# Kernel tuning notes

Measured on AMD Instinct MI355X. Metric: run time of the kernel, lower is better.

## Reference

```python
import jax, jax.numpy as jnp
import numpy as np

TRIANGLE_TABLE = jnp.array([
    [-1, -1, -1, -1, -1, -1], [1, 0, 2, -1, -1, -1], [4, 0, 3, -1, -1, -1],
    [1, 4, 2, 1, 3, 4], [3, 1, 5, -1, -1, -1], [2, 3, 0, 2, 5, 3],
    [1, 4, 0, 1, 5, 4], [4, 2, 5, -1, -1, -1], [4, 5, 2, -1, -1, -1],
    [4, 1, 0, 4, 5, 1], [3, 2, 0, 3, 5, 2], [1, 3, 5, -1, -1, -1],
    [4, 1, 2, 4, 3, 1], [3, 0, 4, -1, -1, -1], [2, 0, 1, -1, -1, -1],
    [-1, -1, -1, -1, -1, -1]], dtype=jnp.int32)
NUM_TRI_TABLE = jnp.array([0, 1, 1, 2, 1, 2, 2, 1, 1, 2, 2, 1, 2, 1, 1, 0], dtype=jnp.int32)
BASE_TET_EDGES = jnp.array([0, 1, 0, 2, 0, 3, 1, 2, 1, 3, 2, 3], dtype=jnp.int32)

NUM_VERTS = 500_000
NUM_TETS = 2_000_000


def setup_inputs() -> dict:
    key = jax.random.key(0)
    k1, k2, k3 = jax.random.split(key, 3)
    pos_nx3 = jax.random.normal(k1, (NUM_VERTS, 3), dtype=jnp.float32)
    sdf_n = jax.random.normal(k2, (NUM_VERTS,), dtype=jnp.float32)
    tet_fx4 = jax.random.randint(k3, (NUM_TETS, 4), 0, NUM_VERTS)
    return {"pos_nx3": pos_nx3, "sdf_n": sdf_n, "tet_fx4": tet_fx4}


def _map_uv(face_gidx, max_idx):
    N = int(np.ceil(np.sqrt((max_idx + 1) // 2)))
    lin = jnp.linspace(0.0, 1.0 - 1.0 / N, N, dtype=jnp.float32)
    tex_y, tex_x = jnp.meshgrid(lin, lin, indexing='ij')
    pad = 0.9 / N
    # (N, N, 8) -> (N*N*4, 2): 4 uv corners per texel
    uvs = jnp.stack([tex_x, tex_y, tex_x + pad, tex_y,
                     tex_x + pad, tex_y + pad, tex_x, tex_y + pad], axis=-1).reshape(-1, 2)
    tet_idx = face_gidx // 2
    x = tet_idx % N
    y = tet_idx // N
    tet_idx = y * N + x
    tri_idx = face_gidx % 2
    uv_idx = jnp.stack([tet_idx * 4, tet_idx * 4 + tri_idx + 1,
                        tet_idx * 4 + tri_idx + 2], axis=-1).reshape(-1, 3)
    return uvs, uv_idx


def reference(pos_nx3, sdf_n, tet_fx4):
    # --- topology extraction (non-differentiable, data-dependent shapes; eager) ---
    occ_n = sdf_n > 0                                  # (N,)
    occ_fx4 = occ_n[tet_fx4]                           # (F, 4)
    occ_sum = occ_fx4.sum(-1)
    valid = (occ_sum > 0) & (occ_sum < 4)              # surface-crossing tets
    tets_v = tet_fx4[valid]                            # (Fv, 4)

    e = tets_v[:, BASE_TET_EDGES].reshape(-1, 2)       # (Fv*6, 2)
    e = jnp.stack([jnp.minimum(e[:, 0], e[:, 1]),
                   jnp.maximum(e[:, 0], e[:, 1])], axis=-1)  # sorted edges
    unique_edges, idx_map = jnp.unique(e, axis=0, return_inverse=True)
    idx_map = idx_map.reshape(-1)

    mask_edges = occ_n[unique_edges].sum(-1) == 1      # edges crossing surface
    mapping = jnp.where(mask_edges, jnp.cumsum(mask_edges) - 1, -1)
    idx_map = mapping[idx_map].reshape(-1, 6)          # (Fv, 6) per-tet edge->vert id
    interp_v = unique_edges[mask_edges]                # (E, 2)

    # --- differentiable vertex interpolation ---
    p = pos_nx3[interp_v]                              # (E, 2, 3)
    signs = jnp.array([[1.0], [-1.0]], dtype=pos_nx3.dtype)
    s = sdf_n[interp_v][..., None] * signs             # (E, 2, 1), second negated
    w = jnp.flip(s, axis=1) / s.sum(1, keepdims=True)
    verts = (p * w).sum(1)                             # (E, 3)

    # --- triangulation via lookup table ---
    v_id = jnp.array([1, 2, 4, 8], dtype=jnp.int32)
    tetindex = (occ_fx4[valid].astype(jnp.int32) * v_id).sum(-1)  # (Fv,)
    ntri = NUM_TRI_TABLE[tetindex]
    m1 = ntri == 1
    m2 = ntri == 2
    f1 = jnp.take_along_axis(idx_map[m1], TRIANGLE_TABLE[tetindex[m1]][:, :3], axis=1).reshape(-1, 3)
    f2 = jnp.take_along_axis(idx_map[m2], TRIANGLE_TABLE[tetindex[m2]][:, :6], axis=1).reshape(-1, 3)
    faces = jnp.concatenate([f1, f2], axis=0)

    num_tets = tet_fx4.shape[0]
    tet_gidx = jnp.arange(num_tets)[valid]
    g2 = tet_gidx[m2] * 2
    face_gidx = jnp.concatenate([tet_gidx[m1] * 2,
                                 jnp.stack([g2, g2 + 1], axis=-1).reshape(-1)], axis=0)
    uvs, uv_idx = _map_uv(face_gidx, num_tets * 2)
    return verts, faces, uvs, uv_idx
```

## Files before the change

kernel.cpp:

```cpp
#include <hip/hip_runtime.h>
#include <stdint.h>
#include <math.h>

#define SB 256
#define SI 8
#define SCHUNK (SB*SI)
#define C2 2048
#define LDSN (C2 + 256)
#define HEADBIT 0x40000000u
#define VMASK   0x3FFFFFFFu

__constant__ int c_tri[16][6] = {
  {-1,-1,-1,-1,-1,-1},{1,0,2,-1,-1,-1},{4,0,3,-1,-1,-1},{1,4,2,1,3,4},
  {3,1,5,-1,-1,-1},{2,3,0,2,5,3},{1,4,0,1,5,4},{4,2,5,-1,-1,-1},
  {4,5,2,-1,-1,-1},{4,1,0,4,5,1},{3,2,0,3,5,2},{1,3,5,-1,-1,-1},
  {4,1,2,4,3,1},{3,0,4,-1,-1,-1},{2,0,1,-1,-1,-1},{-1,-1,-1,-1,-1,-1}};
__constant__ int c_ntri[16] = {0,1,1,2,1,2,2,1,1,2,2,1,2,1,1,0};
__constant__ int c_ea[6] = {0,0,0,1,1,2};
__constant__ int c_eb[6] = {1,2,3,2,3,3};

__global__ void k_classify(const int4* __restrict__ tet, const float* __restrict__ sdf,
                           uint8_t* __restrict__ tetidx, int* __restrict__ bucketCnt,
                           ushort4* __restrict__ stash, int nt) {
  int t = blockIdx.x * blockDim.x + threadIdx.x;
  if (t >= nt) return;
  int4 v = tet[t];
  int ids[4] = {v.x, v.y, v.z, v.w};
  int bits = 0;
#pragma unroll
  for (int i = 0; i < 4; i++) bits |= (sdf[ids[i]] > 0.0f) ? (1 << i) : 0;
  tetidx[t] = (uint8_t)bits;
  if (c_ntri[bits] == 0) return;
  int los[4];
  int c = 0;
#pragma unroll
  for (int e = 0; e < 6; e++) {
    int a = c_ea[e], b = c_eb[e];
    if ((((bits >> a) ^ (bits >> b)) & 1) == 0) continue;
    int va = ids[a], vb = ids[b];
    los[c++] = va < vb ? va : vb;
  }
  unsigned short st[4] = {0, 0, 0, 0};
  unsigned done = 0;
#pragma unroll
  for (int i = 0; i < 4; i++) {
    if (i >= c || (done & (1u << i))) continue;
    int cnt = 1;
#pragma unroll
    for (int j = 1; j < 4; j++)
      if (i + j < c && los[i + j] == los[i]) cnt++;
    int base = atomicAdd(&bucketCnt[los[i]], cnt);
    int k = 0;
#pragma unroll
    for (int j = 0; j < 4; j++) {
      if (i + j < c && los[i + j] == los[i]) {
        st[i + j] = (unsigned short)(base + k);
        k++;
        done |= 1u << (i + j);
      }
    }
  }
  stash[t] = make_ushort4(st[0], st[1], st[2], st[3]);
}

__device__ inline unsigned long long blkExclU64(unsigned long long val, unsigned long long* sh) {
  int tid = threadIdx.x;
  sh[tid] = val; __syncthreads();
  for (int st = 1; st < SB; st <<= 1) {
    unsigned long long add = (tid >= st) ? sh[tid - st] : 0ull;
    __syncthreads();
    sh[tid] += add;
    __syncthreads();
  }
  return sh[tid] - val;
}
__device__ inline int blkExclI32(int val, int* sh) {
  int tid = threadIdx.x;
  sh[tid] = val; __syncthreads();
  for (int st = 1; st < SB; st <<= 1) {
    int add = (tid >= st) ? sh[tid - st] : 0;
    __syncthreads();
    sh[tid] += add;
    __syncthreads();
  }
  return sh[tid] - val;
}

__global__ void k_pass1(const uint8_t* __restrict__ tetidx, int nt,
                        const int* __restrict__ bucketCnt, int nv,
                        unsigned long long* __restrict__ btU, int* __restrict__ btI, int nb_t) {
  __shared__ unsigned long long shU[SB];
  int* shI = (int*)shU;
  if ((int)blockIdx.x < nb_t) {
    int base = blockIdx.x * SCHUNK + threadIdx.x * SI;
    unsigned long long s = 0;
    for (int k = 0; k < SI; k++) {
      int i = base + k;
      if (i < nt) {
        int n3 = c_ntri[tetidx[i]];
        s += (n3 == 1 ? 1ull : 0ull) + (n3 == 2 ? (1ull << 32) : 0ull);
      }
    }
    shU[threadIdx.x] = s; __syncthreads();
    for (int st = SB / 2; st > 0; st >>= 1) {
      if (threadIdx.x < st) shU[threadIdx.x] += shU[threadIdx.x + st];
      __syncthreads();
    }
    if (threadIdx.x == 0) btU[blockIdx.x] = shU[0];
  } else {
    int bid = blockIdx.x - nb_t;
    int base = bid * SCHUNK + threadIdx.x * SI;
    int s = 0;
    for (int k = 0; k < SI; k++) { int i = base + k; if (i < nv) s += bucketCnt[i]; }
    shI[threadIdx.x] = s; __syncthreads();
    for (int st = SB / 2; st > 0; st >>= 1) {
      if (threadIdx.x < st) shI[threadIdx.x] += shI[threadIdx.x + st];
      __syncthreads();
    }
    if (threadIdx.x == 0) btI[bid] = shI[0];
  }
}

__global__ void k_scanmid(unsigned long long* __restrict__ btU, int nbU,
                          int* __restrict__ btI, int nbI, int* __restrict__ scal) {
  __shared__ unsigned long long shU[SB];
  __shared__ unsigned long long carryU;
  int* shI = (int*)shU;
  __shared__ int carryI;
  if (blockIdx.x == 0) {
    if (threadIdx.x == 0) carryU = 0;
    __syncthreads();
    for (int base = 0; base < nbU; base += SB) {
      int i = base + threadIdx.x;
      unsigned long long v = (i < nbU) ? btU[i] : 0ull;
      unsigned long long ex = blkExclU64(v, shU);
      unsigned long long carry = carryU;
      if (i < nbU) btU[i] = carry + ex;
      __syncthreads();
      if (threadIdx.x == SB - 1) carryU = carry + ex + v;
      __syncthreads();
    }
    if (threadIdx.x == 0) {
      scal[0] = (int)(carryU & 0xffffffffull);
      scal[1] = (int)(carryU >> 32);
    }
  } else {
    if (threadIdx.x == 0) carryI = 0;
    __syncthreads();
    for (int base = 0; base < nbI; base += SB) {
      int i = base + threadIdx.x;
      int v = (i < nbI) ? btI[i] : 0;
      int ex = blkExclI32(v, shI);
      int carry = carryI;
      if (i < nbI) btI[i] = carry + ex;
      __syncthreads();
      if (threadIdx.x == SB - 1) carryI = carry + ex + v;
      __syncthreads();
    }
    if (threadIdx.x == 0) scal[2] = carryI;
  }
}

__global__ void k_pass3(const uint8_t* __restrict__ tetidx, int nt,
                        const int* __restrict__ bucketCnt, int nv,
                        const unsigned long long* __restrict__ btU, const int* __restrict__ btI,
                        const int* __restrict__ scal,
                        unsigned* __restrict__ rowIdx, int* __restrict__ bucketOff,
                        int nb_t) {
  __shared__ unsigned long long shU[SB];
  int* shI = (int*)shU;
  if ((int)blockIdx.x < nb_t) {
    int M1 = scal[0];
    int base = blockIdx.x * SCHUNK + threadIdx.x * SI;
    unsigned long long vals[SI];
    int n3s[SI];
    unsigned long long s = 0;
    for (int k = 0; k < SI; k++) {
      int i = base + k;
      unsigned long long v = 0;
      int n3 = 0;
      if (i < nt) {
        n3 = c_ntri[tetidx[i]];
        v = (n3 == 1 ? 1ull : 0ull) + (n3 == 2 ? (1ull << 32) : 0ull);
      }
      n3s[k] = n3;
      vals[k] = s; s += v;
    }
    unsigned long long thrOff = blkExclU64(s, shU);
    unsigned long long off = btU[blockIdx.x] + thrOff;
    for (int k = 0; k < SI; k++) {
      int i = base + k;
      if (i < nt) {
        unsigned long long r = off + vals[k];
        unsigned row = (n3s[k] == 1) ? (unsigned)(r & 0xffffffffull)
                                     : (unsigned)(M1 + 2 * (int)(r >> 32));
        rowIdx[i] = row;
      }
    }
  } else {
    int bid = blockIdx.x - nb_t;
    int base = bid * SCHUNK + threadIdx.x * SI;
    int vals[SI];
    int s = 0;
    for (int k = 0; k < SI; k++) {
      int i = base + k;
      int v = (i < nv) ? bucketCnt[i] : 0;
      vals[k] = s; s += v;
    }
    int thrOff = blkExclI32(s, shI);
    int off = btI[bid] + thrOff;
    for (int k = 0; k < SI; k++) {
      int i = base + k;
      if (i < nv) bucketOff[i] = off + vals[k];
    }
  }
}

__global__ void k_i32scan1(const int* __restrict__ src, int* __restrict__ bt, int n) {
  __shared__ int sh[SB];
  int base = blockIdx.x * SCHUNK + threadIdx.x * SI;
  int s = 0;
  for (int k = 0; k < SI; k++) { int i = base + k; if (i < n) s += src[i]; }
  sh[threadIdx.x] = s; __syncthreads();
  for (int st = SB / 2; st > 0; st >>= 1) {
    if (threadIdx.x < st) sh[threadIdx.x] += sh[threadIdx.x + st];
    __syncthreads();
  }
  if (threadIdx.x == 0) bt[blockIdx.x] = sh[0];
}

__global__ void k_uscanblk(int* __restrict__ bt, int nb, int* __restrict__ scal, int uvsElems) {
  __shared__ int sh[SB];
  __shared__ int carrySh;
  if (threadIdx.x == 0) carrySh = 0;
  __syncthreads();
  for (int base = 0; base < nb; base += SB) {
    int i = base + threadIdx.x;
    int v = (i < nb) ? bt[i] : 0;
    int ex = blkExclI32(v, sh);
    int carry = carrySh;
    if (i < nb) bt[i] = carry + ex;
    __syncthreads();
    if (threadIdx.x == SB - 1) carrySh = carry + ex + v;
    __syncthreads();
  }
  if (threadIdx.x == 0) {
    int E = carrySh;
    scal[3] = E;
    int M1 = scal[0], M2 = scal[1];
    int F = M1 + 2 * M2;
    scal[4] = 3 * E;
    scal[5] = 3 * E + 3 * F;
    scal[6] = scal[5] + uvsElems;
  }
}

__global__ void k_i32scan3(const int* __restrict__ src, const int* __restrict__ bt,
                           int* __restrict__ dst, int n) {
  __shared__ int sh[SB];
  int base = blockIdx.x * SCHUNK + threadIdx.x * SI;
  int vals[SI];
  int s = 0;
  for (int k = 0; k < SI; k++) {
    int i = base + k;
    int v = (i < n) ? src[i] : 0;
    vals[k] = s; s += v;
  }
  int thrOff = blkExclI32(s, sh);
  int off = bt[blockIdx.x] + thrOff;
  for (int k = 0; k < SI; k++) {
    int i = base + k;
    if (i < n) dst[i] = off + vals[k];
  }
}

__global__ void k_scatter(const int4* __restrict__ tet, const uint8_t* __restrict__ tetidx,
                          const int* __restrict__ bucketOff, const ushort4* __restrict__ stash,
                          unsigned* __restrict__ edges32, int4* __restrict__ stashAbs, int nt) {
  int t = blockIdx.x * blockDim.x + threadIdx.x;
  if (t >= nt) return;
  int bits = tetidx[t];
  if (c_ntri[bits] == 0) return;
  int4 v = tet[t];
  int ids[4] = {v.x, v.y, v.z, v.w};
  ushort4 stv = stash[t];
  unsigned short sta[4] = {stv.x, stv.y, stv.z, stv.w};
  int sa[4] = {0, 0, 0, 0};
  int c = 0;
#pragma unroll
  for (int e = 0; e < 6; e++) {
    int a = c_ea[e], b = c_eb[e];
    if ((((bits >> a) ^ (bits >> b)) & 1) == 0) continue;
    int va = ids[a], vb = ids[b];
    int lo = va < vb ? va : vb;
    int hi = va < vb ? vb : va;
    int abs = bucketOff[lo] + (int)sta[c];
    edges32[abs] = (unsigned)hi;
    sa[c] = abs;
    c++;
  }
  stashAbs[t] = make_int4(sa[0], sa[1], sa[2], sa[3]);
}

__global__ __launch_bounds__(SB) void k_rankuniq(
    const int* __restrict__ bucketOff, const unsigned* __restrict__ edges32,
    unsigned short* __restrict__ hrankArr, unsigned* __restrict__ edgesU,
    int* __restrict__ uniqueCnt, int* __restrict__ tmpHead,
    const int* __restrict__ scal, int nv) {
  __shared__ unsigned sh[LDSN];
  __shared__ unsigned shB[LDSN];
  __shared__ int shVS, shVE;
  int totSlots = scal[2];
  long long s0 = (long long)blockIdx.x * C2;
  long long s1 = s0 + C2;
  if (threadIdx.x == 0) {
    int lo = 0, hi = nv;
    while (lo < hi) { int mid = (lo + hi) >> 1;
      long long key = (long long)bucketOff[mid] + mid;
      if (key < s0) lo = mid + 1; else hi = mid; }
    shVS = lo;
    hi = nv;
    while (lo < hi) { int mid = (lo + hi) >> 1;
      long long key = (long long)bucketOff[mid] + mid;
      if (key < s1) lo = mid + 1; else hi = mid; }
    shVE = lo;
  }
  __syncthreads();
  int vS = shVS, vE = shVE;
  if (vS >= vE) return;
  int occS = bucketOff[vS];
  int occE = (vE < nv) ? bucketOff[vE] : totSlots;
  int cnt = occE - occS;
  if (cnt <= LDSN) {
    for (int v = vS + threadIdx.x; v < vE; v += SB) {
      int o = bucketOff[v];
      int nx = (v + 1 < nv) ? bucketOff[v + 1] : totSlots;
      if (nx > o) {
        unsigned pack = ((unsigned)(o - occS) << 16) | (unsigned)(nx - occS);
        for (int k = o; k < nx; k++) shB[k - occS] = pack;
      }
    }
    for (int i = threadIdx.x; i < cnt; i += SB) sh[i] = edges32[occS + i];
    __syncthreads();
    for (int i = threadIdx.x; i < cnt; i += SB) {
      int lb = (int)(shB[i] >> 16);
      unsigned myv = sh[i] & VMASK;
      bool head = true;
      for (int k = lb; k < i; k++)
        if (((sh[k] ^ myv) & VMASK) == 0) { head = false; break; }
      if (head) sh[i] = myv | HEADBIT;
    }
    __syncthreads();
    for (int i = threadIdx.x; i < cnt; i += SB) {
      unsigned b = shB[i];
      int lb = (int)(b >> 16), le = (int)(b & 0xffffu);
      unsigned w0 = sh[i];
      unsigned myv = w0 & VMASK;
      int rank = 0;
      for (int k = lb; k < le; k++) {
        unsigned w = sh[k];
        rank += ((w & HEADBIT) != 0u && (w & VMASK) < myv) ? 1 : 0;
      }
      hrankArr[occS + i] = (unsigned short)rank;
      if (w0 & HEADBIT) edgesU[occS + lb + rank] = myv;
    }
    for (int v = vS + threadIdx.x; v < vE; v += SB) {
      int o = bucketOff[v];
      int nx = (v + 1 < nv) ? bucketOff[v + 1] : totSlots;
      int u = 0;
      for (int k = o - occS; k < nx - occS; k++) u += (sh[k] & HEADBIT) ? 1 : 0;
      uniqueCnt[v] = u;
    }
  } else {
    for (int v = vS + threadIdx.x; v < vE; v += SB) {
      int o = bucketOff[v];
      int nx = (v + 1 < nv) ? bucketOff[v + 1] : totSlots;
      int n = nx - o;
      if (n <= 0) { uniqueCnt[v] = 0; continue; }
      for (int j = 0; j < n; j++) {
        unsigned myv = edges32[o + j];
        int head = 1;
        for (int k = 0; k < j; k++) if (edges32[o + k] == myv) { head = 0; break; }
        tmpHead[o + j] = head;
      }
      int u = 0;
      for (int j = 0; j < n; j++) {
        unsigned myv = edges32[o + j];
        int rank = 0;
        for (int k = 0; k < n; k++)
          rank += (tmpHead[o + k] && edges32[o + k] < myv) ? 1 : 0;
        hrankArr[o + j] = (unsigned short)rank;
        if (tmpHead[o + j]) { edgesU[o + rank] = myv; u++; }
      }
      uniqueCnt[v] = u;
    }
  }
}

__global__ __launch_bounds__(SB) void k_verts(
    const int* __restrict__ bucketOff, const int* __restrict__ uniqueOff,
    const unsigned short* __restrict__ hrankArr, const unsigned* __restrict__ edgesU,
    unsigned* __restrict__ grank, const float* __restrict__ pos, const float* __restrict__ sdf,
    const int* __restrict__ scal, float* __restrict__ out, int nv) {
  __shared__ int shUO[SB + 1];
  __shared__ int shBO[SB + 1];
  int v0 = blockIdx.x * SB;
  int totSlots = scal[2];
  int E = scal[3];
  for (int j = threadIdx.x; j <= SB; j += SB) {
    int gv = v0 + j;
    shUO[j] = (gv < nv) ? uniqueOff[gv] : E;
    shBO[j] = (gv < nv) ? bucketOff[gv] : totSlots;
  }
  __syncthreads();
  int v = v0 + threadIdx.x;
  if (v < nv) {
    int boff = shBO[threadIdx.x];
    int bend = shBO[threadIdx.x + 1];
    int uoff = shUO[threadIdx.x];
    for (int k = boff; k < bend; k++) grank[k] = (unsigned)(uoff + (int)hrankArr[k]);
  }
  int Ustart = shUO[0];
  int Utot = shUO[SB] - Ustart;
  for (int i = threadIdx.x; i < Utot; i += SB) {
    int gi = Ustart + i;
    int lo = 0, hi = SB;
    while (hi - lo > 1) { int mid = (lo + hi) >> 1; if (shUO[mid] <= gi) lo = mid; else hi = mid; }
    int rhat = gi - shUO[lo];
    int hiV = (int)edgesU[shBO[lo] + rhat];
    int loV = v0 + lo;
    float s0 = sdf[loV];
    float ns1 = -sdf[hiV];
    float denom = s0 + ns1;
    float w0 = ns1 / denom;
    float w1 = s0 / denom;
    out[3 * gi + 0] = pos[3 * loV + 0] * w0 + pos[3 * hiV + 0] * w1;
    out[3 * gi + 1] = pos[3 * loV + 1] * w0 + pos[3 * hiV + 1] * w1;
    out[3 * gi + 2] = pos[3 * loV + 2] * w0 + pos[3 * hiV + 2] * w1;
  }
}

__global__ void k_face(const uint8_t* __restrict__ tetidx, const unsigned* __restrict__ rowIdx,
                       const int* __restrict__ scal, const int4* __restrict__ stashAbs,
                       const unsigned* __restrict__ grank, float* __restrict__ out, int nt) {
  int t = blockIdx.x * blockDim.x + threadIdx.x;
  if (t >= nt) return;
  int bits = tetidx[t];
  int nt3 = c_ntri[bits];
  if (nt3 == 0) return;
  int4 sabs = stashAbs[t];
  int sa[4] = {sabs.x, sabs.y, sabs.z, sabs.w};
  int rk[6];
  int c = 0;
#pragma unroll
  for (int e = 0; e < 6; e++) {
    int a = c_ea[e], b = c_eb[e];
    if ((((bits >> a) ^ (bits >> b)) & 1) == 0) continue;
    rk[e] = (int)grank[sa[c++]];
  }
  int row = (int)rowIdx[t];
  int facesOff = scal[4], uvidxOff = scal[6];
  float* f = out + facesOff + (size_t)3 * row;
  int npos = 3 * nt3;
  for (int p = 0; p < npos; p++) f[p] = (float)rk[c_tri[bits][p]];
  float* o = out + uvidxOff + (size_t)3 * row;
  float bt4 = (float)(4 * t);
  o[0] = bt4; o[1] = bt4 + 1.0f; o[2] = bt4 + 2.0f;
  if (nt3 == 2) { o[3] = bt4; o[4] = bt4 + 2.0f; o[5] = bt4 + 3.0f; }
}

__global__ void k_uvs(const int* __restrict__ scal, float* __restrict__ out, int N) {
  int i = blockIdx.x * blockDim.x + threadIdx.x;
  int total = N * N;
  if (i >= total) return;
  int ty = i / N, tx = i - ty * N;
  float x = (float)tx / (float)N;
  float y = (float)ty / (float)N;
  float pad = (float)(0.9 / (double)N);
  float* o = out + scal[5] + (size_t)i * 8;
  float4 a = make_float4(x, y, x + pad, y);
  float4 b = make_float4(x + pad, y + pad, x, y + pad);
  *(float4*)(o) = a;
  *(float4*)(o + 4) = b;
}

extern "C" void kernel_launch(void* const* d_in, const int* in_sizes, int n_in,
                              void* d_out, int out_size, void* d_ws, size_t ws_size,
                              hipStream_t stream) {
  const float* pos = (const float*)d_in[0];
  const float* sdf = (const float*)d_in[1];
  const int* tet = (const int*)d_in[2];
  int nv = in_sizes[1];
  int nt = in_sizes[2] / 4;

  char* w = (char*)d_ws;
  size_t off = 0;
  auto A = [&](size_t bytes) -> char* {
    off = (off + 255) & ~(size_t)255;
    char* p = w + off;
    off += bytes;
    return p;
  };
  int* scal = (int*)A(64 * sizeof(int));
  uint8_t* tetidx = (uint8_t*)A((size_t)nt);
  unsigned* rowIdx = (unsigned*)A((size_t)nt * 4);
  int* bucketCnt = (int*)A((size_t)nv * 4);
  int* bucketOff = (int*)A((size_t)nv * 4);
  int* uniqueCnt = (int*)A((size_t)nv * 4);
  int* uniqueOff = (int*)A((size_t)nv * 4);
  ushort4* stash = (ushort4*)A((size_t)nt * 8);
  int4* stashAbs = (int4*)A((size_t)nt * 16);
  unsigned short* hrankArr = (unsigned short*)A((size_t)nt * 4 * 2);
  unsigned* grank = (unsigned*)A((size_t)nt * 4 * 4);
  unsigned* edges32 = (unsigned*)A((size_t)nt * 4 * 4);
  unsigned* edgesU = (unsigned*)A((size_t)nt * 4 * 4);
  int* tmpHead = (int*)A((size_t)nt * 4 * 4);
  unsigned long long* blockTotU = (unsigned long long*)A(8 * 4096);
  int* blockTotI = (int*)A(4 * 4096);

  hipMemsetAsync(bucketCnt, 0, (size_t)nv * 4, stream);

  int nb_t = (nt + SCHUNK - 1) / SCHUNK;
  int nb_v = (nv + SCHUNK - 1) / SCHUNK;
  int nbv_verts = (nv + SB - 1) / SB;
  long long maxKey = (long long)nt * 4 + nv;
  int nb_rank = (int)((maxKey + C2 - 1) / C2) + 1;

  k_classify<<<(nt + 255) / 256, 256, 0, stream>>>((const int4*)tet, sdf, tetidx, bucketCnt,
                                                   stash, nt);

  k_pass1<<<nb_t + nb_v, SB, 0, stream>>>(tetidx, nt, bucketCnt, nv, blockTotU, blockTotI, nb_t);
  k_scanmid<<<2, SB, 0, stream>>>(blockTotU, nb_t, blockTotI, nb_v, scal);
  k_pass3<<<nb_t + nb_v, SB, 0, stream>>>(tetidx, nt, bucketCnt, nv, blockTotU, blockTotI,
                                          scal, rowIdx, bucketOff, nb_t);

  k_scatter<<<(nt + 255) / 256, 256, 0, stream>>>((const int4*)tet, tetidx, bucketOff,
                                                  stash, edges32, stashAbs, nt);

  k_rankuniq<<<nb_rank, SB, 0, stream>>>(bucketOff, edges32, hrankArr, edgesU,
                                         uniqueCnt, tmpHead, scal, nv);

  long long maxidx = (long long)nt * 2;
  int N = (int)ceil(sqrt((double)((maxidx + 1) / 2)));
  int uvsElems = N * N * 8;

  k_i32scan1<<<nb_v, SB, 0, stream>>>(uniqueCnt, blockTotI, nv);
  k_uscanblk<<<1, SB, 0, stream>>>(blockTotI, nb_v, scal, uvsElems);
  k_i32scan3<<<nb_v, SB, 0, stream>>>(uniqueCnt, blockTotI, uniqueOff, nv);

  k_verts<<<nbv_verts, SB, 0, stream>>>(bucketOff, uniqueOff, hrankArr, edgesU, grank,
                                        pos, sdf, scal, (float*)d_out, nv);
  k_face<<<(nt + 255) / 256, 256, 0, stream>>>(tetidx, rowIdx, scal, stashAbs, grank,
                                               (float*)d_out, nt);
  k_uvs<<<(N * N + 255) / 256, 256, 0, stream>>>(scal, (float*)d_out, N);
}
```

Baseline: 658.4 us.

## Privatize edge bucket counters per XCD to keep atomics in local L2

```diff
diff --git a/kernel.cpp b/kernel.cpp
--- a/kernel.cpp
+++ b/kernel.cpp
@@ -9,6 +9,8 @@
 #define LDSN (C2 + 256)
 #define HEADBIT 0x40000000u
 #define VMASK   0x3FFFFFFFu
+#define NXCD 8
+#define SLOTMASK 0x1fffu
 
 __constant__ int c_tri[16][6] = {
   {-1,-1,-1,-1,-1,-1},{1,0,2,-1,-1,-1},{4,0,3,-1,-1,-1},{1,4,2,1,3,4},
@@ -20,8 +22,12 @@
 __constant__ int c_eb[6] = {1,2,3,2,3,3};
 
 __global__ void k_classify(const int4* __restrict__ tet, const float* __restrict__ sdf,
-                           uint8_t* __restrict__ tetidx, int* __restrict__ bucketCnt,
-                           ushort4* __restrict__ stash, int nt) {
+                           uint8_t* __restrict__ tetidx, int* __restrict__ xoff,
+                           ushort4* __restrict__ stash, int nt, int nv) {
+  unsigned xcc;
+  asm volatile("s_getreg_b32 %0, hwreg(HW_REG_XCC_ID)" : "=s"(xcc));
+  xcc &= 7;
+  int* myCnt = xoff + (size_t)xcc * nv;
   int t = blockIdx.x * blockDim.x + threadIdx.x;
   if (t >= nt) return;
   int4 v = tet[t];
@@ -42,6 +48,7 @@
   }
   unsigned short st[4] = {0, 0, 0, 0};
   unsigned done = 0;
+  unsigned short xtag = (unsigned short)(xcc << 13);
 #pragma unroll
   for (int i = 0; i < 4; i++) {
     if (i >= c || (done & (1u << i))) continue;
@@ -49,18 +56,32 @@
 #pragma unroll
     for (int j = 1; j < 4; j++)
       if (i + j < c && los[i + j] == los[i]) cnt++;
-    int base = atomicAdd(&bucketCnt[los[i]], cnt);
+    int base = __hip_atomic_fetch_add(&myCnt[los[i]], cnt,
+                                      __ATOMIC_RELAXED, __HIP_MEMORY_SCOPE_WORKGROUP);
     int k = 0;
 #pragma unroll
     for (int j = 0; j < 4; j++) {
       if (i + j < c && los[i + j] == los[i]) {
-        st[i + j] = (unsigned short)(base + k);
+        st[i + j] = (unsigned short)((base + k) | xtag);
         k++;
         done |= 1u << (i + j);
       }
     }
   }
   stash[t] = make_ushort4(st[0], st[1], st[2], st[3]);
+}
+
+__global__ void k_xcdoff(int* __restrict__ xoff, int* __restrict__ bucketCnt, int nv) {
+  int v = blockIdx.x * blockDim.x + threadIdx.x;
+  if (v >= nv) return;
+  int run = 0;
+#pragma unroll
+  for (int x = 0; x < NXCD; x++) {
+    int c = xoff[(size_t)x * nv + v];
+    xoff[(size_t)x * nv + v] = run;
+    run += c;
+  }
+  bucketCnt[v] = run;
 }
 
 __device__ inline unsigned long long blkExclU64(unsigned long long val, unsigned long long* sh) {
@@ -166,7 +187,7 @@
                         const unsigned long long* __restrict__ btU, const int* __restrict__ btI,
                         const int* __restrict__ scal,
                         unsigned* __restrict__ rowIdx, int* __restrict__ bucketOff,
-                        int nb_t) {
+                        int* __restrict__ xoff, int nb_t) {
   __shared__ unsigned long long shU[SB];
   int* shI = (int*)shU;
   if ((int)blockIdx.x < nb_t) {
@@ -211,7 +232,12 @@
     int off = btI[bid] + thrOff;
     for (int k = 0; k < SI; k++) {
       int i = base + k;
-      if (i < nv) bucketOff[i] = off + vals[k];
+      if (i < nv) {
+        int val = off + vals[k];
+        bucketOff[i] = val;
+#pragma unroll
+        for (int x = 0; x < NXCD; x++) xoff[(size_t)x * nv + i] += val;
+      }
     }
   }
 }
@@ -275,8 +301,9 @@
 }
 
 __global__ void k_scatter(const int4* __restrict__ tet, const uint8_t* __restrict__ tetidx,
-                          const int* __restrict__ bucketOff, const ushort4* __restrict__ stash,
-                          unsigned* __restrict__ edges32, int4* __restrict__ stashAbs, int nt) {
+                          const int* __restrict__ xoff, const ushort4* __restrict__ stash,
+                          unsigned* __restrict__ edges32, int4* __restrict__ stashAbs,
+                          int nt, int nv) {
   int t = blockIdx.x * blockDim.x + threadIdx.x;
   if (t >= nt) return;
   int bits = tetidx[t];
@@ -294,7 +321,10 @@
     int va = ids[a], vb = ids[b];
     int lo = va < vb ? va : vb;
     int hi = va < vb ? vb : va;
-    int abs = bucketOff[lo] + (int)sta[c];
+    unsigned sv = sta[c];
+    int xcd = (int)(sv >> 13);
+    int slot = (int)(sv & SLOTMASK);
+    int abs = xoff[(size_t)xcd * nv + lo] + slot;
     edges32[abs] = (unsigned)hi;
     sa[c] = abs;
     c++;
@@ -504,6 +534,7 @@
   int* scal = (int*)A(64 * sizeof(int));
   uint8_t* tetidx = (uint8_t*)A((size_t)nt);
   unsigned* rowIdx = (unsigned*)A((size_t)nt * 4);
+  int* xoff = (int*)A((size_t)NXCD * nv * 4);
   int* bucketCnt = (int*)A((size_t)nv * 4);
   int* bucketOff = (int*)A((size_t)nv * 4);
   int* uniqueCnt = (int*)A((size_t)nv * 4);
@@ -518,7 +549,7 @@
   unsigned long long* blockTotU = (unsigned long long*)A(8 * 4096);
   int* blockTotI = (int*)A(4 * 4096);
 
-  hipMemsetAsync(bucketCnt, 0, (size_t)nv * 4, stream);
+  hipMemsetAsync(xoff, 0, (size_t)NXCD * nv * 4, stream);
 
   int nb_t = (nt + SCHUNK - 1) / SCHUNK;
   int nb_v = (nv + SCHUNK - 1) / SCHUNK;
@@ -526,16 +557,17 @@
   long long maxKey = (long long)nt * 4 + nv;
   int nb_rank = (int)((maxKey + C2 - 1) / C2) + 1;
 
-  k_classify<<<(nt + 255) / 256, 256, 0, stream>>>((const int4*)tet, sdf, tetidx, bucketCnt,
-                                                   stash, nt);
+  k_classify<<<(nt + 255) / 256, 256, 0, stream>>>((const int4*)tet, sdf, tetidx, xoff,
+                                                   stash, nt, nv);
+  k_xcdoff<<<(nv + 255) / 256, 256, 0, stream>>>(xoff, bucketCnt, nv);
 
   k_pass1<<<nb_t + nb_v, SB, 0, stream>>>(tetidx, nt, bucketCnt, nv, blockTotU, blockTotI, nb_t);
   k_scanmid<<<2, SB, 0, stream>>>(blockTotU, nb_t, blockTotI, nb_v, scal);
   k_pass3<<<nb_t + nb_v, SB, 0, stream>>>(tetidx, nt, bucketCnt, nv, blockTotU, blockTotI,
-                                          scal, rowIdx, bucketOff, nb_t);
-
-  k_scatter<<<(nt + 255) / 256, 256, 0, stream>>>((const int4*)tet, tetidx, bucketOff,
-                                                  stash, edges32, stashAbs, nt);
+                                          scal, rowIdx, bucketOff, xoff, nb_t);
+
+  k_scatter<<<(nt + 255) / 256, 256, 0, stream>>>((const int4*)tet, tetidx, xoff,
+                                                  stash, edges32, stashAbs, nt, nv);
 
   k_rankuniq<<<nb_rank, SB, 0, stream>>>(bucketOff, edges32, hrankArr, edgesU,
                                          uniqueCnt, tmpHead, scal, nv);
```

Result: slower. 689.9 us (+4.8%).
